# Performance work log

Hardware: AMD Instinct MI355X
Metric: run time of the kernel (lower is better)

The kernel has to match this reference:

```python
import jax, jax.numpy as jnp
import numpy as np

N = 20000        # nodes
E = 640000       # edges
D = 128          # embed_dim
L = 3            # num_layers
NUM_PROTEINS_MASK = 21
BN_EPS = 1e-5


def _batchnorm(x, gamma, beta):
    # training-mode BatchNorm1d: biased batch statistics over axis 0
    mu = jnp.mean(x, axis=0)
    var = jnp.mean((x - mu) ** 2, axis=0)
    return (x - mu) * jax.lax.rsqrt(var + BN_EPS) * gamma + beta


def setup_inputs() -> dict:
    key = jax.random.key(0)
    ks = jax.random.split(key, 20)
    s = 0.05
    return {
        "x_tokens": jax.random.randint(ks[0], (N,), 0, NUM_PROTEINS_MASK),
        "edge_index": jax.random.randint(ks[1], (2, E), 0, N),
        "edge_attr": jax.random.normal(ks[2], (E, D), jnp.float32),
        "emb": jax.random.normal(ks[3], (NUM_PROTEINS_MASK, D), jnp.float32) * s,
        "ee_W": jax.random.normal(ks[4], (L, D, D), jnp.float32) * s,
        "ee_b": jnp.zeros((L, D), jnp.float32),
        "W1": jax.random.normal(ks[5], (L, D, 2 * D), jnp.float32) * s,
        "b1": jnp.zeros((L, 2 * D), jnp.float32),
        "bn1_g": jnp.ones((L, 2 * D), jnp.float32),
        "bn1_b": jnp.zeros((L, 2 * D), jnp.float32),
        "W2": jax.random.normal(ks[6], (L, 2 * D, D), jnp.float32) * s,
        "b2": jnp.zeros((L, D), jnp.float32),
        "eps_p": jnp.zeros((L,), jnp.float32),
        "bn_g": jnp.ones((L, D), jnp.float32),
        "bn_b": jnp.zeros((L, D), jnp.float32),
    }


def reference(x_tokens, edge_index, edge_attr, emb, ee_W, ee_b, W1, b1,
              bn1_g, bn1_b, W2, b2, eps_p, bn_g, bn_b):
    src = edge_index[0]  # x_j is gathered from edge_index[0] (PyG source_to_target)
    dst = edge_index[1]
    h = emb[x_tokens]  # [N, D]
    for l in range(L):
        # GINConv: edge encode, gather-message-scatter
        ea = edge_attr @ ee_W[l] + ee_b[l]                      # [E, D]
        msg = jax.nn.relu(h[src] + ea)                          # [E, D]
        agg = jax.ops.segment_sum(msg, dst, num_segments=N)     # [N, D]
        z = (1.0 + eps_p[l]) * h + agg
        # MLP: Linear -> BN -> ReLU -> Linear
        z = _batchnorm(z @ W1[l] + b1[l], bn1_g[l], bn1_b[l])
        z = jax.nn.relu(z)
        h = z @ W2[l] + b2[l]
        # outer BatchNorm; ReLU except last layer; dropout p=0 -> identity
        h = _batchnorm(h, bn_g[l], bn_b[l])
        if l < L - 1:
            h = jax.nn.relu(h)
    return h
```

## Files before the change

kernel.cpp:

```cpp
#include <hip/hip_runtime.h>
#include <stdint.h>

#define NN 20000
#define EE 640000
#define DDIM 128
#define D2 256
#define NLAY 3
#define BN_EPS 1e-5f

typedef short bf16x8 __attribute__((ext_vector_type(8)));
typedef float f32x4 __attribute__((ext_vector_type(4)));

__device__ __forceinline__ short f2bf(float f) {
    uint32_t u = __float_as_uint(f);
    u += 0x7fff + ((u >> 16) & 1);
    return (short)(u >> 16);
}
__device__ __forceinline__ float bf2f(uint32_t u16) {
    return __uint_as_float(u16 << 16);
}

__global__ __launch_bounds__(256) void k_embed(const int* __restrict__ tok,
                                               const float* __restrict__ emb,
                                               float* __restrict__ h) {
    int gid = blockIdx.x * 256 + threadIdx.x;
    int r = gid >> 5;
    int c4 = gid & 31;
    int t = tok[r];
    ((float4*)h)[gid] = ((const float4*)emb)[t * 32 + c4];
}

__global__ __launch_bounds__(256) void k_hist(const int* __restrict__ ei, int* __restrict__ counts) {
    int e = blockIdx.x * 256 + threadIdx.x;
    atomicAdd(&counts[ei[EE + e]], 1);
}

__global__ __launch_bounds__(1024) void k_scan(const int* __restrict__ counts, int* __restrict__ cursor) {
    __shared__ int buf[NN];
    __shared__ int part[1024];
    int t = threadIdx.x;
    for (int i = t; i < NN; i += 1024) buf[i] = counts[i];
    __syncthreads();
    int base = t * 20;
    int s = 0;
    #pragma unroll
    for (int i = 0; i < 20; i++) {
        int idx = base + i;
        if (idx < NN) s += buf[idx];
    }
    part[t] = s;
    __syncthreads();
    for (int off = 1; off < 1024; off <<= 1) {
        int v = (t >= off) ? part[t - off] : 0;
        __syncthreads();
        part[t] += v;
        __syncthreads();
    }
    int run = part[t] - s;
    #pragma unroll
    for (int i = 0; i < 20; i++) {
        int idx = base + i;
        if (idx < NN) { int c = buf[idx]; buf[idx] = run; run += c; }
    }
    __syncthreads();
    for (int i = t; i < NN; i += 1024) cursor[i] = buf[i];
}

__global__ __launch_bounds__(256) void k_scatter(const int* __restrict__ ei,
                                                 int* __restrict__ cursor,
                                                 int* __restrict__ perm,
                                                 int* __restrict__ rank) {
    int e = blockIdx.x * 256 + threadIdx.x;
    int d = ei[EE + e];
    int pos = atomicAdd(&cursor[d], 1);
    perm[pos] = e;
    rank[e] = pos;
}

__global__ __launch_bounds__(256) void k_permute2(const float* __restrict__ edge_attr,
                                                  const int* __restrict__ ei,
                                                  const int* __restrict__ rank,
                                                  short* __restrict__ ea_bf,
                                                  int* __restrict__ srcs,
                                                  int* __restrict__ dsts) {
    int gid = blockIdx.x * 256 + threadIdx.x;
    int e = gid >> 5, c4 = gid & 31;
    float4 v = ((const float4*)edge_attr)[gid];
    int pos = rank[e];
    short4 b;
    b.x = f2bf(v.x); b.y = f2bf(v.y); b.z = f2bf(v.z); b.w = f2bf(v.w);
    ((short4*)ea_bf)[(size_t)pos * 32 + c4] = b;
    if (c4 == 0) { srcs[pos] = ei[e]; dsts[pos] = ei[EE + e]; }
}

__global__ __launch_bounds__(256) void k_prepw(const float* __restrict__ src,
                                               short* __restrict__ dst,
                                               int K, int Nc, int total) {
    int gid = blockIdx.x * 256 + threadIdx.x;
    if (gid >= total) return;
    int per = K * Nc;
    int l = gid / per;
    int rem = gid - l * per;
    int k = rem / Nc;
    int n = rem - k * Nc;
    dst[(l * Nc + n) * K + k] = f2bf(src[gid]);
}

__global__ __launch_bounds__(256) void k_edge3(const short* __restrict__ ea_bf,
                                               const int* __restrict__ srcs,
                                               const int* __restrict__ dsts,
                                               const short* __restrict__ WtL,
                                               const float* __restrict__ ebL,
                                               const float* __restrict__ hbase,
                                               const float* __restrict__ st2,
                                               const float* __restrict__ g2,
                                               const float* __restrict__ b2v,
                                               int lazy,
                                               float* __restrict__ agg) {
    __shared__ __align__(16) short sW[128 * 136];
    __shared__ __align__(16) short sOutB[64 * 132];
    __shared__ int sSrc[64], sDst[64];
    int tid = threadIdx.x;
    int tile = blockIdx.x;

    if (tid < 64) {
        sSrc[tid] = srcs[tile * 64 + tid];
        sDst[tid] = dsts[tile * 64 + tid];
    }
    const uint2* wg = (const uint2*)WtL;
    #pragma unroll
    for (int i = 0; i < 16; i++) {
        int idx = tid + i * 256;
        uint2 v = wg[idx];
        int n = idx >> 5, k4 = (idx & 31) << 2;
        *(uint2*)&sW[n * 136 + k4] = v;
    }
    int lane = tid & 63, wv = tid >> 6;
    int l15 = lane & 15, quad = lane >> 4;
    int r0 = wv * 16;
    const short* abase = ea_bf + ((size_t)(tile * 64 + r0 + l15)) * 128 + quad * 8;
    bf16x8 a[4];
    #pragma unroll
    for (int kt = 0; kt < 4; kt++) a[kt] = *(const bf16x8*)(abase + kt * 32);
    __syncthreads();

    f32x4 acc[8];
    #pragma unroll
    for (int i = 0; i < 8; i++) acc[i] = (f32x4){0.f, 0.f, 0.f, 0.f};
    #pragma unroll
    for (int kt = 0; kt < 4; kt++) {
        #pragma unroll
        for (int nt = 0; nt < 8; nt++) {
            bf16x8 b = *(const bf16x8*)&sW[(nt * 16 + l15) * 136 + kt * 32 + quad * 8];
            acc[nt] = __builtin_amdgcn_mfma_f32_16x16x32_bf16(a[kt], b, acc[nt], 0, 0, 0);
        }
    }
    #pragma unroll
    for (int nt = 0; nt < 8; nt++) {
        float ebv = ebL[nt * 16 + l15];
        #pragma unroll
        for (int reg = 0; reg < 4; reg++)
            sOutB[(r0 + quad * 4 + reg) * 132 + nt * 16 + l15] = f2bf(acc[nt][reg] + ebv);
    }
    __syncthreads();

    {
        int c2 = tid & 63;
        int c = c2 * 2;
        int rb = tid >> 6;
        float s0 = 0.f, s1 = 0.f, t0 = 0.f, t1 = 0.f;
        if (lazy) {
            float inv_n = 1.f / (float)NN;
            float mu0 = st2[c] * inv_n,     mu1 = st2[c + 1] * inv_n;
            float va0 = st2[128 + c] * inv_n - mu0 * mu0;
            float va1 = st2[129 + c] * inv_n - mu1 * mu1;
            s0 = g2[c] * rsqrtf(va0 + BN_EPS);     t0 = b2v[c] - mu0 * s0;
            s1 = g2[c + 1] * rsqrtf(va1 + BN_EPS); t1 = b2v[c + 1] - mu1 * s1;
        }
        #pragma unroll
        for (int i = 0; i < 16; i++) {
            int r = rb + i * 4;
            float2 hv = *(const float2*)&hbase[(size_t)sSrc[r] * DDIM + c];
            float h0, h1;
            if (lazy) {
                h0 = fmaxf(hv.x * s0 + t0, 0.f);
                h1 = fmaxf(hv.y * s1 + t1, 0.f);
            } else {
                h0 = hv.x; h1 = hv.y;
            }
            uint32_t pp = *(uint32_t*)&sOutB[r * 132 + c];
            float m0 = fmaxf(bf2f(pp & 0xffffu) + h0, 0.f);
            float m1 = fmaxf(bf2f(pp >> 16) + h1, 0.f);
            uint32_t po = (uint32_t)(uint16_t)f2bf(m0) | ((uint32_t)(uint16_t)f2bf(m1) << 16);
            *(uint32_t*)&sOutB[r * 132 + c] = po;
        }
    }
    __syncthreads();
    int c = tid & 127;
    int rbeg = (tid >> 7) * 32;
    float s = 0.f;
    int cur = sDst[rbeg];
    for (int r = rbeg; r < rbeg + 32; r++) {
        int d = sDst[r];
        if (d != cur) { atomicAdd(&agg[(size_t)cur * DDIM + c], s); s = 0.f; cur = d; }
        uint32_t raw = *(const uint16_t*)&sOutB[r * 132 + c];
        s += bf2f(raw);
    }
    atomicAdd(&agg[(size_t)cur * DDIM + c], s);
}

__global__ __launch_bounds__(256) void k_edge_g(const float* __restrict__ edge_attr,
                                                const short* __restrict__ WtL,
                                                const float* __restrict__ ebL,
                                                const float* __restrict__ h,
                                                const int* __restrict__ ei,
                                                const int* __restrict__ perm,
                                                float* __restrict__ agg) {
    __shared__ __align__(16) short sW[128 * 136];
    __shared__ __align__(16) char sU[64 * 132 * 4];
    __shared__ int sSrc[64], sDst[64], sEdge[64];
    short* sA = (short*)sU;
    float* sOut = (float*)sU;
    int tid = threadIdx.x;
    int tile = blockIdx.x;
    if (tid < 64) {
        int e = perm[tile * 64 + tid];
        sEdge[tid] = e;
        sSrc[tid] = ei[e];
        sDst[tid] = ei[EE + e];
    }
    const uint2* wg = (const uint2*)WtL;
    #pragma unroll
    for (int i = 0; i < 16; i++) {
        int idx = tid + i * 256;
        uint2 v = wg[idx];
        int n = idx >> 5, k4 = (idx & 31) << 2;
        *(uint2*)&sW[n * 136 + k4] = v;
    }
    __syncthreads();
    #pragma unroll
    for (int i = 0; i < 8; i++) {
        int idx = tid + i * 256;
        int r = idx >> 5, c4 = idx & 31;
        float4 v = ((const float4*)edge_attr)[sEdge[r] * 32 + c4];
        short4 b;
        b.x = f2bf(v.x); b.y = f2bf(v.y); b.z = f2bf(v.z); b.w = f2bf(v.w);
        *(short4*)&sA[r * 136 + (c4 << 2)] = b;
    }
    __syncthreads();
    int lane = tid & 63, wv = tid >> 6;
    int l15 = lane & 15, quad = lane >> 4;
    int r0 = wv * 16;
    f32x4 acc[8];
    #pragma unroll
    for (int i = 0; i < 8; i++) acc[i] = (f32x4){0.f, 0.f, 0.f, 0.f};
    #pragma unroll
    for (int kt = 0; kt < 4; kt++) {
        bf16x8 a = *(const bf16x8*)&sA[(r0 + l15) * 136 + kt * 32 + quad * 8];
        #pragma unroll
        for (int nt = 0; nt < 8; nt++) {
            bf16x8 b = *(const bf16x8*)&sW[(nt * 16 + l15) * 136 + kt * 32 + quad * 8];
            acc[nt] = __builtin_amdgcn_mfma_f32_16x16x32_bf16(a, b, acc[nt], 0, 0, 0);
        }
    }
    __syncthreads();
    #pragma unroll
    for (int nt = 0; nt < 8; nt++)
        #pragma unroll
        for (int reg = 0; reg < 4; reg++)
            sOut[(r0 + quad * 4 + reg) * 132 + nt * 16 + l15] = acc[nt][reg];
    __syncthreads();
    #pragma unroll
    for (int i = 0; i < 32; i++) {
        int idx = tid + i * 256;
        int r = idx >> 7, c = idx & 127;
        float v = sOut[r * 132 + c] + ebL[c] + h[(size_t)sSrc[r] * DDIM + c];
        sOut[r * 132 + c] = fmaxf(v, 0.f);
    }
    __syncthreads();
    int c = tid & 127;
    int rbeg = (tid >> 7) * 32;
    float s = 0.f;
    int cur = sDst[rbeg];
    for (int r = rbeg; r < rbeg + 32; r++) {
        int d = sDst[r];
        if (d != cur) { atomicAdd(&agg[(size_t)cur * DDIM + c], s); s = 0.f; cur = d; }
        s += sOut[r * 132 + c];
    }
    atomicAdd(&agg[(size_t)cur * DDIM + c], s);
}

__global__ __launch_bounds__(256) void k_gemm1z(const float* __restrict__ hbase,
                                                const float* __restrict__ st2,
                                                const float* __restrict__ g2,
                                                const float* __restrict__ b2v,
                                                int lazy,
                                                const float* __restrict__ agg,
                                                const float* __restrict__ epsP, int l,
                                                const short* __restrict__ W1tL,
                                                float* __restrict__ zz,
                                                float* __restrict__ stats) {
    __shared__ __align__(16) short sB[128 * 136];
    __shared__ __align__(16) short sA[64 * 136];
    int tid = threadIdx.x;
    int tile = blockIdx.x;
    int half = blockIdx.y;
    float e1 = 1.f + epsP[l];
    const uint2* bg = (const uint2*)W1tL + (size_t)half * 128 * 32;
    #pragma unroll
    for (int i = 0; i < 16; i++) {
        int idx = tid + i * 256;
        uint2 v = bg[idx];
        int n = idx >> 5, k4 = (idx & 31) << 2;
        *(uint2*)&sB[n * 136 + k4] = v;
    }
    {
        int c4 = tid & 31;
        int c = c4 * 4;
        float scv[4] = {0.f, 0.f, 0.f, 0.f}, shv[4] = {0.f, 0.f, 0.f, 0.f};
        if (lazy) {
            float inv_n = 1.f / (float)NN;
            #pragma unroll
            for (int j = 0; j < 4; j++) {
                float mu = st2[c + j] * inv_n;
                float var = st2[128 + c + j] * inv_n - mu * mu;
                float sc = g2[c + j] * rsqrtf(var + BN_EPS);
                scv[j] = sc;
                shv[j] = b2v[c + j] - mu * sc;
            }
        }
        #pragma unroll
        for (int i = 0; i < 8; i++) {
            int idx = tid + i * 256;
            int r = idx >> 5;
            int gr = tile * 64 + r;
            short4 o = {0, 0, 0, 0};
            if (gr < NN) {
                float4 hv = ((const float4*)hbase)[gr * 32 + c4];
                if (lazy) {
                    hv.x = fmaxf(hv.x * scv[0] + shv[0], 0.f);
                    hv.y = fmaxf(hv.y * scv[1] + shv[1], 0.f);
                    hv.z = fmaxf(hv.z * scv[2] + shv[2], 0.f);
                    hv.w = fmaxf(hv.w * scv[3] + shv[3], 0.f);
                }
                float4 av = ((const float4*)agg)[gr * 32 + c4];
                o.x = f2bf(e1 * hv.x + av.x);
                o.y = f2bf(e1 * hv.y + av.y);
                o.z = f2bf(e1 * hv.z + av.z);
                o.w = f2bf(e1 * hv.w + av.w);
            }
            *(short4*)&sA[r * 136 + c] = o;
        }
    }
    __syncthreads();
    int lane = tid & 63, wv = tid >> 6;
    int l15 = lane & 15, quad = lane >> 4;
    int r0 = wv * 16;
    f32x4 acc[8];
    #pragma unroll
    for (int i = 0; i < 8; i++) acc[i] = (f32x4){0.f, 0.f, 0.f, 0.f};
    #pragma unroll
    for (int kt = 0; kt < 4; kt++) {
        bf16x8 a = *(const bf16x8*)&sA[(r0 + l15) * 136 + kt * 32 + quad * 8];
        #pragma unroll
        for (int nt = 0; nt < 8; nt++) {
            bf16x8 b = *(const bf16x8*)&sB[(nt * 16 + l15) * 136 + kt * 32 + quad * 8];
            acc[nt] = __builtin_amdgcn_mfma_f32_16x16x32_bf16(a, b, acc[nt], 0, 0, 0);
        }
    }
    int grb = tile * 64 + r0 + quad * 4;
    #pragma unroll
    for (int nt = 0; nt < 8; nt++) {
        int col = half * 128 + nt * 16 + l15;
        float s = 0.f, s2 = 0.f;
        #pragma unroll
        for (int reg = 0; reg < 4; reg++) {
            int gr = grb + reg;
            float v = acc[nt][reg];
            s += v; s2 += v * v;
            if (gr < NN) zz[(size_t)gr * D2 + col] = v;
        }
        s += __shfl_xor(s, 16);  s += __shfl_xor(s, 32);
        s2 += __shfl_xor(s2, 16); s2 += __shfl_xor(s2, 32);
        if (quad == 0) {
            atomicAdd(&stats[col], s);
            atomicAdd(&stats[D2 + col], s2);
        }
    }
}

__global__ __launch_bounds__(256) void k_gemm2s(const float* __restrict__ zz,
                                                const short* __restrict__ W2tL,
                                                const float* __restrict__ st1,
                                                const float* __restrict__ g1,
                                                const float* __restrict__ b1v,
                                                float* __restrict__ h_pre,
                                                float* __restrict__ stats) {
    __shared__ __align__(16) short sB[64 * 264];
    __shared__ __align__(16) short sA[64 * 264];
    __shared__ float sSc[256], sSh[256];
    int tid = threadIdx.x;
    int tile = blockIdx.x;
    int half = blockIdx.y;
    {
        float inv_n = 1.f / (float)NN;
        float mu = st1[tid] * inv_n;
        float var = st1[256 + tid] * inv_n - mu * mu;
        float sc = g1[tid] * rsqrtf(var + BN_EPS);
        sSc[tid] = sc;
        sSh[tid] = b1v[tid] - mu * sc;
    }
    const uint2* bg = (const uint2*)W2tL + (size_t)half * 64 * 64;
    #pragma unroll
    for (int i = 0; i < 16; i++) {
        int idx = tid + i * 256;
        uint2 v = bg[idx];
        int n = idx >> 6, k4 = (idx & 63) << 2;
        *(uint2*)&sB[n * 264 + k4] = v;
    }
    __syncthreads();
    #pragma unroll
    for (int i = 0; i < 16; i++) {
        int idx = tid + i * 256;
        int r = idx >> 6, c4q = idx & 63;
        int c4 = c4q << 2;
        int gr = tile * 64 + r;
        short4 o = {0, 0, 0, 0};
        if (gr < NN) {
            float4 v = ((const float4*)zz)[gr * 64 + c4q];
            o.x = f2bf(fmaxf(v.x * sSc[c4 + 0] + sSh[c4 + 0], 0.f));
            o.y = f2bf(fmaxf(v.y * sSc[c4 + 1] + sSh[c4 + 1], 0.f));
            o.z = f2bf(fmaxf(v.z * sSc[c4 + 2] + sSh[c4 + 2], 0.f));
            o.w = f2bf(fmaxf(v.w * sSc[c4 + 3] + sSh[c4 + 3], 0.f));
        }
        *(short4*)&sA[r * 264 + c4] = o;
    }
    __syncthreads();
    int lane = tid & 63, wv = tid >> 6;
    int l15 = lane & 15, quad = lane >> 4;
    int r0 = wv * 16;
    f32x4 acc[4];
    #pragma unroll
    for (int i = 0; i < 4; i++) acc[i] = (f32x4){0.f, 0.f, 0.f, 0.f};
    #pragma unroll
    for (int kt = 0; kt < 8; kt++) {
        bf16x8 a = *(const bf16x8*)&sA[(r0 + l15) * 264 + kt * 32 + quad * 8];
        #pragma unroll
        for (int nt = 0; nt < 4; nt++) {
            bf16x8 b = *(const bf16x8*)&sB[(nt * 16 + l15) * 264 + kt * 32 + quad * 8];
            acc[nt] = __builtin_amdgcn_mfma_f32_16x16x32_bf16(a, b, acc[nt], 0, 0, 0);
        }
    }
    int grb = tile * 64 + r0 + quad * 4;
    #pragma unroll
    for (int nt = 0; nt < 4; nt++) {
        int col = half * 64 + nt * 16 + l15;
        float s = 0.f, s2 = 0.f;
        #pragma unroll
        for (int reg = 0; reg < 4; reg++) {
            int gr = grb + reg;
            float v = acc[nt][reg];
            s += v; s2 += v * v;
            if (gr < NN) h_pre[(size_t)gr * DDIM + col] = v;
        }
        s += __shfl_xor(s, 16);  s += __shfl_xor(s, 32);
        s2 += __shfl_xor(s2, 16); s2 += __shfl_xor(s2, 32);
        if (quad == 0) {
            atomicAdd(&stats[col], s);
            atomicAdd(&stats[DDIM + col], s2);
        }
    }
}

__global__ __launch_bounds__(256) void k_bn2(const float* __restrict__ h_pre,
                                             const float* __restrict__ st2,
                                             const float* __restrict__ g2,
                                             const float* __restrict__ b2v,
                                             int do_relu, float* __restrict__ dst) {
    int gid = blockIdx.x * 256 + threadIdx.x;
    int c0 = (gid & 31) << 2;
    float inv_n = 1.f / (float)NN;
    float4 v = ((const float4*)h_pre)[gid];
    float o[4];
    #pragma unroll
    for (int j = 0; j < 4; j++) {
        float mu = st2[c0 + j] * inv_n;
        float var = st2[128 + c0 + j] * inv_n - mu * mu;
        float sc = g2[c0 + j] * rsqrtf(var + BN_EPS);
        float sh = b2v[c0 + j] - mu * sc;
        float x = (&v.x)[j] * sc + sh;
        o[j] = do_relu ? fmaxf(x, 0.f) : x;
    }
    float4 ov = make_float4(o[0], o[1], o[2], o[3]);
    ((float4*)dst)[gid] = ov;
}

extern "C" void kernel_launch(void* const* d_in, const int* in_sizes, int n_in,
                              void* d_out, int out_size, void* d_ws, size_t ws_size,
                              hipStream_t stream) {
    const int*   tok       = (const int*)d_in[0];
    const int*   ei        = (const int*)d_in[1];
    const float* edge_attr = (const float*)d_in[2];
    const float* emb       = (const float*)d_in[3];
    const float* eeW       = (const float*)d_in[4];
    const float* eeB       = (const float*)d_in[5];
    const float* W1        = (const float*)d_in[6];
    const float* bn1g      = (const float*)d_in[8];
    const float* bn1b      = (const float*)d_in[9];
    const float* W2        = (const float*)d_in[10];
    const float* epsP      = (const float*)d_in[12];
    const float* bng       = (const float*)d_in[13];
    const float* bnb       = (const float*)d_in[14];
    float* out = (float*)d_out;

    char* ws = (char*)d_ws;
    size_t off = 0;
    auto alloc = [&](size_t bytes) -> char* {
        off = (off + 511) & ~(size_t)511;
        char* p = ws + off;
        off += bytes;
        return p;
    };
    float* h      = (float*)alloc((size_t)NN * DDIM * 4);
    float* aggs   = (float*)alloc(((size_t)NN * DDIM + 512) * 4);
    float* agg    = aggs;
    float* stats1 = aggs + (size_t)NN * DDIM;
    float* zz     = (float*)alloc((size_t)NN * D2 * 4);
    float* h_pre  = (float*)alloc((size_t)NN * DDIM * 4);
    int*   perm   = (int*)alloc((size_t)EE * 4);
    int*   rank   = (int*)alloc((size_t)EE * 4);
    int*   counts = (int*)alloc((size_t)NN * 4);
    int*   cursor = (int*)alloc((size_t)NN * 4);
    int*   srcs   = (int*)alloc((size_t)EE * 4);
    int*   dsts   = (int*)alloc((size_t)EE * 4);
    short* WtE    = (short*)alloc((size_t)NLAY * 128 * 128 * 2);
    short* W1t    = (short*)alloc((size_t)NLAY * 128 * 256 * 2);
    short* W2t    = (short*)alloc((size_t)NLAY * 256 * 128 * 2);
    float* stats2 = (float*)alloc(512 * 4);
    short* ea_bf  = (short*)alloc((size_t)EE * DDIM * 2);
    bool big = (off <= ws_size);
    (void)in_sizes; (void)n_in; (void)out_size;

    hipMemsetAsync(counts, 0, (size_t)NN * 4, stream);
    {
        int t1 = NLAY * 128 * 128;
        k_prepw<<<(t1 + 255) / 256, 256, 0, stream>>>(eeW, WtE, 128, 128, t1);
        int t2 = NLAY * 128 * 256;
        k_prepw<<<(t2 + 255) / 256, 256, 0, stream>>>(W1, W1t, 128, 256, t2);
        int t3 = NLAY * 256 * 128;
        k_prepw<<<(t3 + 255) / 256, 256, 0, stream>>>(W2, W2t, 256, 128, t3);
    }
    k_embed<<<2500, 256, 0, stream>>>(tok, emb, h);
    k_hist<<<2500, 256, 0, stream>>>(ei, counts);
    k_scan<<<1, 1024, 0, stream>>>(counts, cursor);
    k_scatter<<<2500, 256, 0, stream>>>(ei, cursor, perm, rank);
    if (big) {
        k_permute2<<<EE * 32 / 256, 256, 0, stream>>>(edge_attr, ei, rank, ea_bf, srcs, dsts);
    }

    for (int l = 0; l < NLAY; l++) {
        hipMemsetAsync(aggs, 0, ((size_t)NN * DDIM + 512) * 4, stream);
        float* st2cur  = stats2 + (l & 1) * 256;
        float* st2prev = stats2 + ((l + 1) & 1) * 256;
        hipMemsetAsync(st2cur, 0, 256 * 4, stream);
        int lazy = (big && l > 0) ? 1 : 0;
        const float* hb  = lazy ? h_pre : h;
        int lp = (l > 0) ? (l - 1) : 0;
        const float* g2p = bng + (size_t)lp * 128;
        const float* b2p = bnb + (size_t)lp * 128;
        if (big) {
            k_edge3<<<EE / 64, 256, 0, stream>>>(ea_bf, srcs, dsts,
                                                 WtE + (size_t)l * 128 * 128,
                                                 eeB + (size_t)l * 128,
                                                 hb, st2prev, g2p, b2p, lazy, agg);
        } else {
            k_edge_g<<<EE / 64, 256, 0, stream>>>(edge_attr, WtE + (size_t)l * 128 * 128,
                                                  eeB + (size_t)l * 128, h, ei, perm, agg);
        }
        k_gemm1z<<<dim3((NN + 63) / 64, 2), 256, 0, stream>>>(hb, st2prev, g2p, b2p, lazy, agg,
                                                              epsP, l,
                                                              W1t + (size_t)l * 128 * 256, zz, stats1);
        k_gemm2s<<<dim3((NN + 63) / 64, 2), 256, 0, stream>>>(zz, W2t + (size_t)l * 256 * 128,
                                                              stats1, bn1g + (size_t)l * 256,
                                                              bn1b + (size_t)l * 256, h_pre, st2cur);
        if (big) {
            if (l == NLAY - 1)
                k_bn2<<<2500, 256, 0, stream>>>(h_pre, st2cur, bng + (size_t)l * 128,
                                                bnb + (size_t)l * 128, 0, out);
        } else {
            k_bn2<<<2500, 256, 0, stream>>>(h_pre, st2cur, bng + (size_t)l * 128,
                                            bnb + (size_t)l * 128, (l < NLAY - 1) ? 1 : 0,
                                            (l == NLAY - 1) ? out : h);
        }
    }
}
```

Baseline: 1.226 ms.

## Amortize edge-weight staging over four tiles, split gemm2 K, merge setup kernels

The edge kernel now handles four 64-edge tiles per block, so the 128x128 bf16 edge-encoder weight is staged into LDS once per four tiles instead of once per tile, and the BN coefficients and bias are hoisted out of the loop. The second MLP GEMM processes K in two halves of 128 with smaller LDS buffers, which lowers shared-memory use per block and may raise occupancy. The three weight-prep launches are merged into one kernel, and the embedding and degree-histogram kernels are fused, cutting launch count. The trade-off is that the edge kernel launches a quarter as many blocks, which may hurt load balance and latency hiding, and the extra barriers per tile serialize work.

```diff
diff --git a/kernel.cpp b/kernel.cpp
--- a/kernel.cpp
+++ b/kernel.cpp
@@ -20,19 +20,17 @@
     return __uint_as_float(u16 << 16);
 }
 
-__global__ __launch_bounds__(256) void k_embed(const int* __restrict__ tok,
-                                               const float* __restrict__ emb,
-                                               float* __restrict__ h) {
+__global__ __launch_bounds__(256) void k_embed_hist(const int* __restrict__ tok,
+                                                    const float* __restrict__ emb,
+                                                    float* __restrict__ h,
+                                                    const int* __restrict__ ei,
+                                                    int* __restrict__ counts) {
     int gid = blockIdx.x * 256 + threadIdx.x;
     int r = gid >> 5;
     int c4 = gid & 31;
     int t = tok[r];
     ((float4*)h)[gid] = ((const float4*)emb)[t * 32 + c4];
-}
-
-__global__ __launch_bounds__(256) void k_hist(const int* __restrict__ ei, int* __restrict__ counts) {
-    int e = blockIdx.x * 256 + threadIdx.x;
-    atomicAdd(&counts[ei[EE + e]], 1);
+    atomicAdd(&counts[ei[EE + gid]], 1);
 }
 
 __global__ __launch_bounds__(1024) void k_scan(const int* __restrict__ counts, int* __restrict__ cursor) {
@@ -93,17 +91,31 @@
     if (c4 == 0) { srcs[pos] = ei[e]; dsts[pos] = ei[EE + e]; }
 }
 
-__global__ __launch_bounds__(256) void k_prepw(const float* __restrict__ src,
-                                               short* __restrict__ dst,
-                                               int K, int Nc, int total) {
+__global__ __launch_bounds__(256) void k_prepw_all(const float* __restrict__ eeW,
+                                                   const float* __restrict__ W1,
+                                                   const float* __restrict__ W2,
+                                                   short* __restrict__ WtE,
+                                                   short* __restrict__ W1t,
+                                                   short* __restrict__ W2t) {
     int gid = blockIdx.x * 256 + threadIdx.x;
-    if (gid >= total) return;
-    int per = K * Nc;
-    int l = gid / per;
-    int rem = gid - l * per;
-    int k = rem / Nc;
-    int n = rem - k * Nc;
-    dst[(l * Nc + n) * K + k] = f2bf(src[gid]);
+    const int T1 = NLAY * 128 * 128;
+    const int T2 = NLAY * 128 * 256;
+    const int T3 = NLAY * 256 * 128;
+    if (gid < T1) {
+        int l = gid / (128 * 128), rem = gid % (128 * 128);
+        int k = rem >> 7, n = rem & 127;
+        WtE[(l * 128 + n) * 128 + k] = f2bf(eeW[gid]);
+    } else if (gid < T1 + T2) {
+        int g = gid - T1;
+        int l = g / (128 * 256), rem = g % (128 * 256);
+        int k = rem >> 8, n = rem & 255;
+        W1t[(l * 256 + n) * 128 + k] = f2bf(W1[g]);
+    } else if (gid < T1 + T2 + T3) {
+        int g = gid - T1 - T2;
+        int l = g / (256 * 128), rem = g % (256 * 128);
+        int k = rem >> 7, n = rem & 127;
+        W2t[(l * 128 + n) * 256 + k] = f2bf(W2[g]);
+    }
 }
 
 __global__ __launch_bounds__(256) void k_edge3(const short* __restrict__ ea_bf,
@@ -121,12 +133,7 @@
     __shared__ __align__(16) short sOutB[64 * 132];
     __shared__ int sSrc[64], sDst[64];
     int tid = threadIdx.x;
-    int tile = blockIdx.x;
-
-    if (tid < 64) {
-        sSrc[tid] = srcs[tile * 64 + tid];
-        sDst[tid] = dsts[tile * 64 + tid];
-    }
+
     const uint2* wg = (const uint2*)WtL;
     #pragma unroll
     for (int i = 0; i < 16; i++) {
@@ -138,75 +145,87 @@
     int lane = tid & 63, wv = tid >> 6;
     int l15 = lane & 15, quad = lane >> 4;
     int r0 = wv * 16;
-    const short* abase = ea_bf + ((size_t)(tile * 64 + r0 + l15)) * 128 + quad * 8;
-    bf16x8 a[4];
-    #pragma unroll
-    for (int kt = 0; kt < 4; kt++) a[kt] = *(const bf16x8*)(abase + kt * 32);
-    __syncthreads();
-
-    f32x4 acc[8];
-    #pragma unroll
-    for (int i = 0; i < 8; i++) acc[i] = (f32x4){0.f, 0.f, 0.f, 0.f};
-    #pragma unroll
-    for (int kt = 0; kt < 4; kt++) {
+
+    float ebv[8];
+    #pragma unroll
+    for (int nt = 0; nt < 8; nt++) ebv[nt] = ebL[nt * 16 + l15];
+
+    int pc2 = tid & 63;
+    int pc = pc2 * 2;
+    int prb = tid >> 6;
+    float ls0 = 0.f, ls1 = 0.f, lt0 = 0.f, lt1 = 0.f;
+    if (lazy) {
+        float inv_n = 1.f / (float)NN;
+        float mu0 = st2[pc] * inv_n,     mu1 = st2[pc + 1] * inv_n;
+        float va0 = st2[128 + pc] * inv_n - mu0 * mu0;
+        float va1 = st2[129 + pc] * inv_n - mu1 * mu1;
+        ls0 = g2[pc] * rsqrtf(va0 + BN_EPS);     lt0 = b2v[pc] - mu0 * ls0;
+        ls1 = g2[pc + 1] * rsqrtf(va1 + BN_EPS); lt1 = b2v[pc + 1] - mu1 * ls1;
+    }
+
+    #pragma unroll 1
+    for (int sub = 0; sub < 4; sub++) {
+        int tile = blockIdx.x * 4 + sub;
+        if (tid < 64) {
+            sSrc[tid] = srcs[tile * 64 + tid];
+            sDst[tid] = dsts[tile * 64 + tid];
+        }
+        const short* abase = ea_bf + ((size_t)(tile * 64 + r0 + l15)) * 128 + quad * 8;
+        bf16x8 a[4];
+        #pragma unroll
+        for (int kt = 0; kt < 4; kt++) a[kt] = *(const bf16x8*)(abase + kt * 32);
+        if (sub == 0) __syncthreads();
+
+        f32x4 acc[8];
+        #pragma unroll
+        for (int i = 0; i < 8; i++) acc[i] = (f32x4){0.f, 0.f, 0.f, 0.f};
+        #pragma unroll
+        for (int kt = 0; kt < 4; kt++) {
+            #pragma unroll
+            for (int nt = 0; nt < 8; nt++) {
+                bf16x8 b = *(const bf16x8*)&sW[(nt * 16 + l15) * 136 + kt * 32 + quad * 8];
+                acc[nt] = __builtin_amdgcn_mfma_f32_16x16x32_bf16(a[kt], b, acc[nt], 0, 0, 0);
+            }
+        }
         #pragma unroll
         for (int nt = 0; nt < 8; nt++) {
-            bf16x8 b = *(const bf16x8*)&sW[(nt * 16 + l15) * 136 + kt * 32 + quad * 8];
-            acc[nt] = __builtin_amdgcn_mfma_f32_16x16x32_bf16(a[kt], b, acc[nt], 0, 0, 0);
-        }
-    }
-    #pragma unroll
-    for (int nt = 0; nt < 8; nt++) {
-        float ebv = ebL[nt * 16 + l15];
-        #pragma unroll
-        for (int reg = 0; reg < 4; reg++)
-            sOutB[(r0 + quad * 4 + reg) * 132 + nt * 16 + l15] = f2bf(acc[nt][reg] + ebv);
-    }
-    __syncthreads();
-
-    {
-        int c2 = tid & 63;
-        int c = c2 * 2;
-        int rb = tid >> 6;
-        float s0 = 0.f, s1 = 0.f, t0 = 0.f, t1 = 0.f;
-        if (lazy) {
-            float inv_n = 1.f / (float)NN;
-            float mu0 = st2[c] * inv_n,     mu1 = st2[c + 1] * inv_n;
-            float va0 = st2[128 + c] * inv_n - mu0 * mu0;
-            float va1 = st2[129 + c] * inv_n - mu1 * mu1;
-            s0 = g2[c] * rsqrtf(va0 + BN_EPS);     t0 = b2v[c] - mu0 * s0;
-            s1 = g2[c + 1] * rsqrtf(va1 + BN_EPS); t1 = b2v[c + 1] - mu1 * s1;
-        }
+            #pragma unroll
+            for (int reg = 0; reg < 4; reg++)
+                sOutB[(r0 + quad * 4 + reg) * 132 + nt * 16 + l15] = f2bf(acc[nt][reg] + ebv[nt]);
+        }
+        __syncthreads();
+
         #pragma unroll
         for (int i = 0; i < 16; i++) {
-            int r = rb + i * 4;
-            float2 hv = *(const float2*)&hbase[(size_t)sSrc[r] * DDIM + c];
+            int r = prb + i * 4;
+            float2 hv = *(const float2*)&hbase[(size_t)sSrc[r] * DDIM + pc];
             float h0, h1;
             if (lazy) {
-                h0 = fmaxf(hv.x * s0 + t0, 0.f);
-                h1 = fmaxf(hv.y * s1 + t1, 0.f);
+                h0 = fmaxf(hv.x * ls0 + lt0, 0.f);
+                h1 = fmaxf(hv.y * ls1 + lt1, 0.f);
             } else {
                 h0 = hv.x; h1 = hv.y;
             }
-            uint32_t pp = *(uint32_t*)&sOutB[r * 132 + c];
+            uint32_t pp = *(uint32_t*)&sOutB[r * 132 + pc];
             float m0 = fmaxf(bf2f(pp & 0xffffu) + h0, 0.f);
             float m1 = fmaxf(bf2f(pp >> 16) + h1, 0.f);
             uint32_t po = (uint32_t)(uint16_t)f2bf(m0) | ((uint32_t)(uint16_t)f2bf(m1) << 16);
-            *(uint32_t*)&sOutB[r * 132 + c] = po;
-        }
-    }
-    __syncthreads();
-    int c = tid & 127;
-    int rbeg = (tid >> 7) * 32;
-    float s = 0.f;
-    int cur = sDst[rbeg];
-    for (int r = rbeg; r < rbeg + 32; r++) {
-        int d = sDst[r];
-        if (d != cur) { atomicAdd(&agg[(size_t)cur * DDIM + c], s); s = 0.f; cur = d; }
-        uint32_t raw = *(const uint16_t*)&sOutB[r * 132 + c];
-        s += bf2f(raw);
-    }
-    atomicAdd(&agg[(size_t)cur * DDIM + c], s);
+            *(uint32_t*)&sOutB[r * 132 + pc] = po;
+        }
+        __syncthreads();
+        int c = tid & 127;
+        int rbeg = (tid >> 7) * 32;
+        float s = 0.f;
+        int cur = sDst[rbeg];
+        for (int r = rbeg; r < rbeg + 32; r++) {
+            int d = sDst[r];
+            if (d != cur) { atomicAdd(&agg[(size_t)cur * DDIM + c], s); s = 0.f; cur = d; }
+            uint32_t raw = *(const uint16_t*)&sOutB[r * 132 + c];
+            s += bf2f(raw);
+        }
+        atomicAdd(&agg[(size_t)cur * DDIM + c], s);
+        if (sub < 3) __syncthreads();
+    }
 }
 
 __global__ __launch_bounds__(256) void k_edge_g(const float* __restrict__ edge_attr,
@@ -396,59 +415,75 @@
                                                 const float* __restrict__ b1v,
                                                 float* __restrict__ h_pre,
                                                 float* __restrict__ stats) {
-    __shared__ __align__(16) short sB[64 * 264];
-    __shared__ __align__(16) short sA[64 * 264];
+    __shared__ __align__(16) short sB[64 * 136];
+    __shared__ __align__(16) short sA[64 * 136];
     __shared__ float sSc[256], sSh[256];
     int tid = threadIdx.x;
     int tile = blockIdx.x;
     int half = blockIdx.y;
-    {
-        float inv_n = 1.f / (float)NN;
-        float mu = st1[tid] * inv_n;
-        float var = st1[256 + tid] * inv_n - mu * mu;
-        float sc = g1[tid] * rsqrtf(var + BN_EPS);
-        sSc[tid] = sc;
-        sSh[tid] = b1v[tid] - mu * sc;
-    }
-    const uint2* bg = (const uint2*)W2tL + (size_t)half * 64 * 64;
-    #pragma unroll
-    for (int i = 0; i < 16; i++) {
-        int idx = tid + i * 256;
-        uint2 v = bg[idx];
-        int n = idx >> 6, k4 = (idx & 63) << 2;
-        *(uint2*)&sB[n * 264 + k4] = v;
-    }
-    __syncthreads();
-    #pragma unroll
-    for (int i = 0; i < 16; i++) {
-        int idx = tid + i * 256;
-        int r = idx >> 6, c4q = idx & 63;
-        int c4 = c4q << 2;
-        int gr = tile * 64 + r;
-        short4 o = {0, 0, 0, 0};
-        if (gr < NN) {
-            float4 v = ((const float4*)zz)[gr * 64 + c4q];
-            o.x = f2bf(fmaxf(v.x * sSc[c4 + 0] + sSh[c4 + 0], 0.f));
-            o.y = f2bf(fmaxf(v.y * sSc[c4 + 1] + sSh[c4 + 1], 0.f));
-            o.z = f2bf(fmaxf(v.z * sSc[c4 + 2] + sSh[c4 + 2], 0.f));
-            o.w = f2bf(fmaxf(v.w * sSc[c4 + 3] + sSh[c4 + 3], 0.f));
-        }
-        *(short4*)&sA[r * 264 + c4] = o;
-    }
-    __syncthreads();
     int lane = tid & 63, wv = tid >> 6;
     int l15 = lane & 15, quad = lane >> 4;
     int r0 = wv * 16;
     f32x4 acc[4];
     #pragma unroll
     for (int i = 0; i < 4; i++) acc[i] = (f32x4){0.f, 0.f, 0.f, 0.f};
-    #pragma unroll
-    for (int kt = 0; kt < 8; kt++) {
-        bf16x8 a = *(const bf16x8*)&sA[(r0 + l15) * 264 + kt * 32 + quad * 8];
-        #pragma unroll
-        for (int nt = 0; nt < 4; nt++) {
-            bf16x8 b = *(const bf16x8*)&sB[(nt * 16 + l15) * 264 + kt * 32 + quad * 8];
-            acc[nt] = __builtin_amdgcn_mfma_f32_16x16x32_bf16(a, b, acc[nt], 0, 0, 0);
+
+    #pragma unroll 1
+    for (int p = 0; p < 2; p++) {
+        if (p == 0) {
+            float inv_n = 1.f / (float)NN;
+            float mu = st1[tid] * inv_n;
+            float var = st1[256 + tid] * inv_n - mu * mu;
+            float sc = g1[tid] * rsqrtf(var + BN_EPS);
+            sSc[tid] = sc;
+            sSh[tid] = b1v[tid] - mu * sc;
+            const uint2* bg = (const uint2*)W2tL + (size_t)half * 64 * 64;
+            #pragma unroll
+            for (int i = 0; i < 8; i++) {
+                int idx = tid + i * 256;
+                int n = idx >> 5, k4q = idx & 31;
+                uint2 v = bg[n * 64 + k4q];
+                *(uint2*)&sB[n * 136 + k4q * 4] = v;
+            }
+            __syncthreads();
+        } else {
+            __syncthreads();
+            const uint2* bg = (const uint2*)W2tL + (size_t)half * 64 * 64 + 32;
+            #pragma unroll
+            for (int i = 0; i < 8; i++) {
+                int idx = tid + i * 256;
+                int n = idx >> 5, k4q = idx & 31;
+                uint2 v = bg[n * 64 + k4q];
+                *(uint2*)&sB[n * 136 + k4q * 4] = v;
+            }
+        }
+        {
+            int c4q = tid & 31;
+            int cb = p * 128 + c4q * 4;
+            #pragma unroll
+            for (int i = 0; i < 8; i++) {
+                int r = (tid >> 5) + i * 8;
+                int gr = tile * 64 + r;
+                short4 o = {0, 0, 0, 0};
+                if (gr < NN) {
+                    float4 v = ((const float4*)zz)[(size_t)gr * 64 + p * 32 + c4q];
+                    o.x = f2bf(fmaxf(v.x * sSc[cb + 0] + sSh[cb + 0], 0.f));
+                    o.y = f2bf(fmaxf(v.y * sSc[cb + 1] + sSh[cb + 1], 0.f));
+                    o.z = f2bf(fmaxf(v.z * sSc[cb + 2] + sSh[cb + 2], 0.f));
+                    o.w = f2bf(fmaxf(v.w * sSc[cb + 3] + sSh[cb + 3], 0.f));
+                }
+                *(short4*)&sA[r * 136 + c4q * 4] = o;
+            }
+        }
+        __syncthreads();
+        #pragma unroll
+        for (int kt = 0; kt < 4; kt++) {
+            bf16x8 a = *(const bf16x8*)&sA[(r0 + l15) * 136 + kt * 32 + quad * 8];
+            #pragma unroll
+            for (int nt = 0; nt < 4; nt++) {
+                bf16x8 b = *(const bf16x8*)&sB[(nt * 16 + l15) * 136 + kt * 32 + quad * 8];
+                acc[nt] = __builtin_amdgcn_mfma_f32_16x16x32_bf16(a, b, acc[nt], 0, 0, 0);
+            }
         }
     }
     int grb = tile * 64 + r0 + quad * 4;
@@ -542,16 +577,8 @@
     (void)in_sizes; (void)n_in; (void)out_size;
 
     hipMemsetAsync(counts, 0, (size_t)NN * 4, stream);
-    {
-        int t1 = NLAY * 128 * 128;
-        k_prepw<<<(t1 + 255) / 256, 256, 0, stream>>>(eeW, WtE, 128, 128, t1);
-        int t2 = NLAY * 128 * 256;
-        k_prepw<<<(t2 + 255) / 256, 256, 0, stream>>>(W1, W1t, 128, 256, t2);
-        int t3 = NLAY * 256 * 128;
-        k_prepw<<<(t3 + 255) / 256, 256, 0, stream>>>(W2, W2t, 256, 128, t3);
-    }
-    k_embed<<<2500, 256, 0, stream>>>(tok, emb, h);
-    k_hist<<<2500, 256, 0, stream>>>(ei, counts);
+    k_prepw_all<<<960, 256, 0, stream>>>(eeW, W1, W2, WtE, W1t, W2t);
+    k_embed_hist<<<2500, 256, 0, stream>>>(tok, emb, h, ei, counts);
     k_scan<<<1, 1024, 0, stream>>>(counts, cursor);
     k_scatter<<<2500, 256, 0, stream>>>(ei, cursor, perm, rank);
     if (big) {
@@ -569,10 +596,10 @@
         const float* g2p = bng + (size_t)lp * 128;
         const float* b2p = bnb + (size_t)lp * 128;
         if (big) {
-            k_edge3<<<EE / 64, 256, 0, stream>>>(ea_bf, srcs, dsts,
-                                                 WtE + (size_t)l * 128 * 128,
-                                                 eeB + (size_t)l * 128,
-                                                 hb, st2prev, g2p, b2p, lazy, agg);
+            k_edge3<<<EE / 256, 256, 0, stream>>>(ea_bf, srcs, dsts,
+                                                  WtE + (size_t)l * 128 * 128,
+                                                  eeB + (size_t)l * 128,
+                                                  hb, st2prev, g2p, b2p, lazy, agg);
         } else {
             k_edge_g<<<EE / 64, 256, 0, stream>>>(edge_attr, WtE + (size_t)l * 128 * 128,
                                                   eeB + (size_t)l * 128, h, ei, perm, agg);
```

Measured after the change: 1.179 ms. 3.8% less time.
